# Optimization experiments

Hardware: AMD Instinct MI355X
Metric: run time of the kernel (lower is better)

The kernel has to match this reference:

```python
import jax, jax.numpy as jnp
import numpy as np


def setup_inputs() -> dict:
    key = jax.random.key(0)
    ks = jax.random.split(key, 5)
    B, S, C = 512, 512, 96
    emissions = jax.random.normal(ks[0], (B, S, C), dtype=jnp.float32)
    tags = jax.random.randint(ks[1], (B, S), 0, C, dtype=jnp.int64)
    masks = jnp.ones((B, S), dtype=bool)
    start_transitions = jax.random.uniform(ks[2], (C,), jnp.float32, -0.1, 0.1)
    end_transitions = jax.random.uniform(ks[3], (C,), jnp.float32, -0.1, 0.1)
    transitions = jax.random.uniform(ks[4], (C, C), jnp.float32, -0.1, 0.1)
    return {
        "emissions": emissions,
        "tags": tags,
        "masks": masks,
        "start_transitions": start_transitions,
        "end_transitions": end_transitions,
        "transitions": transitions,
    }


def _crf_llh(emissions, tags, masks, start_transitions, end_transitions, transitions):
    # to time-major: (S, B, C), (S, B)
    emissions = jnp.swapaxes(emissions, 0, 1)
    tags = jnp.swapaxes(tags, 0, 1)
    masks = jnp.swapaxes(masks, 0, 1)
    S, B, C = emissions.shape
    maskf = masks.astype(emissions.dtype)

    # ---- numerator: score of the gold tag path (fully vectorized over time) ----
    em_scores = jnp.take_along_axis(emissions, tags[:, :, None], axis=2)[:, :, 0]  # (S, B)
    trans_scores = transitions[tags[:-1], tags[1:]]  # (S-1, B)
    score = start_transitions[tags[0]] + em_scores[0]
    score = score + jnp.sum((trans_scores + em_scores[1:]) * maskf[1:], axis=0)
    seq_ends = masks.astype(jnp.int32).sum(axis=0) - 1  # (B,)
    last_tags = tags[seq_ends, jnp.arange(B)]
    numerator = score + end_transitions[last_tags]

    # ---- denominator: forward algorithm (sequential logsumexp recurrence) ----
    alpha0 = start_transitions[None, :] + emissions[0]  # (B, C)

    def step(alpha, inp):
        em_i, m_i = inp  # (B, C), (B,)
        # (B, C_prev, C_next)
        scores = alpha[:, :, None] + transitions[None, :, :] + em_i[:, None, :]
        next_alpha = jax.scipy.special.logsumexp(scores, axis=1)
        alpha = jnp.where(m_i[:, None], next_alpha, alpha)
        return alpha, None

    alpha, _ = jax.lax.scan(step, alpha0, (emissions[1:], masks[1:]))
    denominator = jax.scipy.special.logsumexp(alpha + end_transitions[None, :], axis=1)

    return jnp.mean(numerator - denominator)


def reference(emissions, tags, masks, start_transitions, end_transitions, transitions):
    return _crf_llh(emissions, tags, masks, start_transitions, end_transitions, transitions)
```

## Files before the change

kernel.cpp:

```cpp
#include <hip/hip_runtime.h>
#include <hip/hip_bf16.h>
#include <math.h>


#define BATCH 512
#define SEQ   512
#define NC    96
#define NTHR  128
#define LN2   0.69314718055994531f

typedef __fp16 half2v __attribute__((ext_vector_type(2)));

#define BARRIER() asm volatile("s_waitcnt lgkmcnt(0)\n\ts_barrier" ::: "memory")

#define DPP_STEP_F(v, op, ctrl)                                              \
    v = op(v, __int_as_float(__builtin_amdgcn_update_dpp(                    \
            __float_as_int(v), __float_as_int(v), (ctrl), 0xf, 0xf, false)))

__device__ __forceinline__ float wave_max_all(float v) {
    DPP_STEP_F(v, fmaxf, 0x111);
    DPP_STEP_F(v, fmaxf, 0x112);
    DPP_STEP_F(v, fmaxf, 0x114);
    DPP_STEP_F(v, fmaxf, 0x118);
    DPP_STEP_F(v, fmaxf, 0x142);
    DPP_STEP_F(v, fmaxf, 0x143);
    return __int_as_float(__builtin_amdgcn_readlane(__float_as_int(v), 63));
}
__device__ __forceinline__ float fadd_(float a, float b) { return a + b; }
__device__ __forceinline__ float wave_sum_all(float v) {
    DPP_STEP_F(v, fadd_, 0x111);
    DPP_STEP_F(v, fadd_, 0x112);
    DPP_STEP_F(v, fadd_, 0x114);
    DPP_STEP_F(v, fadd_, 0x118);
    DPP_STEP_F(v, fadd_, 0x142);
    DPP_STEP_F(v, fadd_, 0x143);
    return __int_as_float(__builtin_amdgcn_readlane(__float_as_int(v), 63));
}

__global__ __launch_bounds__(NTHR, 1)
void crf_llh_kernel(const float* __restrict__ em,
                    const int*   __restrict__ tags,
                    const int*   __restrict__ masks,
                    const float* __restrict__ startT,
                    const float* __restrict__ endT,
                    const float* __restrict__ trans,
                    float*       __restrict__ out)
{
    const int b    = blockIdx.x;
    const int tid  = threadIdx.x;
    const int lane = tid & 63;
    const int wid  = tid >> 6;
    const bool active = (tid < NC);
    const int jc = active ? tid : 0;

    __shared__ __align__(16) __fp16 qsh[2][128];
    __shared__ float maxsh[2][2];
    __shared__ float redn[2], redm[2], redd[2];

    const float* em_b    = em    + (size_t)b * SEQ * NC;
    const int*   tags_b  = tags  + b * SEQ;
    const int*   masks_b = masks + b * SEQ;

    half2v ecol[48];
    #pragma unroll
    for (int k = 0; k < 48; ++k) {
        ecol[k] = __builtin_amdgcn_cvt_pkrtz(
            __expf(trans[(2 * k)     * NC + jc]),
            __expf(trans[(2 * k + 1) * NC + jc]));
    }

    const float al0 = startT[jc] + em_b[jc];
    {
        const float wm = wave_max_all(active ? al0 : -1e30f);
        if (lane == 0) maxsh[0][wid] = wm;
    }
    BARRIER();
    const float M0 = fmaxf(maxsh[0][0], maxsh[0][1]);
    float wreg = active ? __expf(al0 - M0) : 0.f;
    qsh[1][tid] = (__fp16)wreg;
    BARRIER();

    int K    = 1;
    int sumk = 0;

    float emA = em_b[1 * NC + jc];
    float emB = em_b[2 * NC + jc];
    float emC = em_b[3 * NC + jc];
    int mkA = masks_b[1], mkB = masks_b[2], mkC = masks_b[3];

    for (int s = 1; s < SEQ; ++s) {
        const int rb = s & 1;
        const int sp = (s + 3 < SEQ) ? (s + 3) : (SEQ - 1);
        const float emN = em_b[sp * NC + jc];
        const int   mkN = masks_b[sp];

        const uint4* q4p = reinterpret_cast<const uint4*>(&qsh[rb][0]);
        uint4 qv[12];
        #pragma unroll
        for (int t = 0; t < 12; ++t) qv[t] = q4p[t];

        float acc[6] = {0.f, 0.f, 0.f, 0.f, 0.f, 0.f};
        #pragma unroll
        for (int t = 0; t < 12; ++t) {
            const half2v qx = __builtin_bit_cast(half2v, qv[t].x);
            const half2v qy = __builtin_bit_cast(half2v, qv[t].y);
            const half2v qz = __builtin_bit_cast(half2v, qv[t].z);
            const half2v qw = __builtin_bit_cast(half2v, qv[t].w);
            acc[(4 * t + 0) % 6] = __builtin_amdgcn_fdot2(qx, ecol[4 * t + 0], acc[(4 * t + 0) % 6], false);
            acc[(4 * t + 1) % 6] = __builtin_amdgcn_fdot2(qy, ecol[4 * t + 1], acc[(4 * t + 1) % 6], false);
            acc[(4 * t + 2) % 6] = __builtin_amdgcn_fdot2(qz, ecol[4 * t + 2], acc[(4 * t + 2) % 6], false);
            acc[(4 * t + 3) % 6] = __builtin_amdgcn_fdot2(qw, ecol[4 * t + 3], acc[(4 * t + 3) % 6], false);
        }
        const float U = ((acc[0] + acc[1]) + (acc[2] + acc[3])) + (acc[4] + acc[5]);

        const float F = __expf(emA);
        float w = ldexpf(U, -(K + 6)) * F;
        if (!active) w = 0.f;
        w = mkA ? w : wreg;
        sumk += mkA ? (K + 6) : 0;
        wreg = w;

        const float wmx = wave_max_all(w);
        if (lane == 0) maxsh[rb][wid] = wmx;
        qsh[rb ^ 1][tid] = (__fp16)w;
        BARRIER();

        const float r = fmaxf(maxsh[rb][0], maxsh[rb][1]);
        K = (int)((__float_as_uint(r) >> 23) & 255u) - 126;

        emA = emB; emB = emC; emC = emN;
        mkA = mkB; mkB = mkC; mkC = mkN;
    }

    const float dv = active ? wreg * __expf(endT[jc]) : 0.f;
    {
        const float ws = wave_sum_all(dv);
        if (lane == 0) redd[wid] = ws;
    }
    __syncthreads();
    const float denom = M0 + (float)sumk * LN2 + __logf(redd[0] + redd[1]);

    float nsum = 0.f, msum = 0.f;
    #pragma unroll
    for (int kk = 0; kk < SEQ / NTHR; ++kk) {
        const int s  = tid + NTHR * kk;
        const int tg = tags_b[s];
        const int mk = masks_b[s];
        msum += mk ? 1.f : 0.f;
        if (s == 0) {
            nsum += startT[tg] + em_b[tg];
        } else if (mk) {
            nsum += trans[tags_b[s - 1] * NC + tg] + em_b[s * NC + tg];
        }
    }
    nsum = wave_sum_all(nsum);
    msum = wave_sum_all(msum);
    if (lane == 0) { redn[wid] = nsum; redm[wid] = msum; }
    __syncthreads();
    if (tid == 0) {
        const float numer = redn[0] + redn[1];
        const int   cnt   = (int)(redm[0] + redm[1]);
        const int   last  = tags_b[cnt - 1];
        atomicAdd(out, (numer + endT[last] - denom) * (1.0f / (float)BATCH));
    }
}

extern "C" void kernel_launch(void* const* d_in, const int* in_sizes, int n_in,
                              void* d_out, int out_size, void* d_ws, size_t ws_size,
                              hipStream_t stream) {
    const float* em     = (const float*)d_in[0];
    const int*   tags   = (const int*)  d_in[1];
    const int*   masks  = (const int*)  d_in[2];
    const float* startT = (const float*)d_in[3];
    const float* endT   = (const float*)d_in[4];
    const float* trans  = (const float*)d_in[5];
    float* out = (float*)d_out;

    (void)hipMemsetAsync(out, 0, sizeof(float), stream);
    crf_llh_kernel<<<BATCH, NTHR, 0, stream>>>(em, tags, masks, startT, endT, trans, out);
}
```

Measured before the change: 402.9 us.

## Fuse timestep pairs via MFMA-built two-step transition matrices in producer warps

Three producer waves use MFMA to build, for each pair of timesteps, the combined matrix E·diag(exp(em))·E in fp16 shared memory, double-buffered. A single consumer wave then applies one matvec per two steps, which halves the serial recurrence length. Masked steps fall back to single-step matvecs. This trades extra parallel MFMA work and fp16 precision loss in the fused matrix for a shorter sequential dependency chain and fewer barriers per step.

After: 426.3 us. 1.06x slower.

```diff
diff --git a/kernel.cpp b/kernel.cpp
--- a/kernel.cpp
+++ b/kernel.cpp
@@ -1,31 +1,28 @@
 #include <hip/hip_runtime.h>
-#include <hip/hip_bf16.h>
 #include <math.h>
 
 
 #define BATCH 512
 #define SEQ   512
 #define NC    96
-#define NTHR  128
+#define NTHR  256
+#define CSTR  120
+#define GHALF (NC * CSTR)
 #define LN2   0.69314718055994531f
 
 typedef __fp16 half2v __attribute__((ext_vector_type(2)));
+typedef __fp16 half8  __attribute__((ext_vector_type(8)));
+typedef float  f32x4  __attribute__((ext_vector_type(4)));
+typedef unsigned int uint2v __attribute__((ext_vector_type(2)));
+typedef unsigned int uint4v __attribute__((ext_vector_type(4)));
 
 #define BARRIER() asm volatile("s_waitcnt lgkmcnt(0)\n\ts_barrier" ::: "memory")
+#define LGKM0()   asm volatile("s_waitcnt lgkmcnt(0)" ::: "memory")
 
 #define DPP_STEP_F(v, op, ctrl)                                              \
     v = op(v, __int_as_float(__builtin_amdgcn_update_dpp(                    \
             __float_as_int(v), __float_as_int(v), (ctrl), 0xf, 0xf, false)))
 
-__device__ __forceinline__ float wave_max_all(float v) {
-    DPP_STEP_F(v, fmaxf, 0x111);
-    DPP_STEP_F(v, fmaxf, 0x112);
-    DPP_STEP_F(v, fmaxf, 0x114);
-    DPP_STEP_F(v, fmaxf, 0x118);
-    DPP_STEP_F(v, fmaxf, 0x142);
-    DPP_STEP_F(v, fmaxf, 0x143);
-    return __int_as_float(__builtin_amdgcn_readlane(__float_as_int(v), 63));
-}
 __device__ __forceinline__ float fadd_(float a, float b) { return a + b; }
 __device__ __forceinline__ float wave_sum_all(float v) {
     DPP_STEP_F(v, fadd_, 0x111);
@@ -36,132 +33,274 @@
     DPP_STEP_F(v, fadd_, 0x143);
     return __int_as_float(__builtin_amdgcn_readlane(__float_as_int(v), 63));
 }
-
-__global__ __launch_bounds__(NTHR, 1)
-void crf_llh_kernel(const float* __restrict__ em,
-                    const int*   __restrict__ tags,
-                    const int*   __restrict__ masks,
-                    const float* __restrict__ startT,
-                    const float* __restrict__ endT,
-                    const float* __restrict__ trans,
-                    float*       __restrict__ out)
+__device__ __forceinline__ float wave_max_all(float v) {
+    DPP_STEP_F(v, fmaxf, 0x111);
+    DPP_STEP_F(v, fmaxf, 0x112);
+    DPP_STEP_F(v, fmaxf, 0x114);
+    DPP_STEP_F(v, fmaxf, 0x118);
+    DPP_STEP_F(v, fmaxf, 0x142);
+    DPP_STEP_F(v, fmaxf, 0x143);
+    return __int_as_float(__builtin_amdgcn_readlane(__float_as_int(v), 63));
+}
+
+__device__ __forceinline__ unsigned bcu(half2v h) { return __builtin_bit_cast(unsigned, h); }
+__device__ __forceinline__ half2v bch(unsigned u) { return __builtin_bit_cast(half2v, u); }
+__device__ __forceinline__ float fdot2_(unsigned a, unsigned b, float c) {
+    return __builtin_amdgcn_fdot2(bch(a), bch(b), c, false);
+}
+
+__device__ __forceinline__ void matvec96(const __fp16* base, const __fp16* st,
+                                         int jj, float& u0, float& u1) {
+    const uint4v* c0 = (const uint4v*)(base + (2 * jj) * CSTR);
+    const uint4v* c1 = (const uint4v*)(base + (2 * jj) * CSTR + CSTR);
+    const uint4v* sp = (const uint4v*)st;
+    uint4v g0[12], g1[12], sv[12];
+    #pragma unroll
+    for (int q = 0; q < 12; ++q) g0[q] = c0[q];
+    #pragma unroll
+    for (int q = 0; q < 12; ++q) g1[q] = c1[q];
+    #pragma unroll
+    for (int q = 0; q < 12; ++q) sv[q] = sp[q];
+    float a0 = 0.f, a1 = 0.f, a2 = 0.f, a3 = 0.f;
+    float b0 = 0.f, b1 = 0.f, b2 = 0.f, b3 = 0.f;
+    #pragma unroll
+    for (int q = 0; q < 12; ++q) {
+        a0 = fdot2_(sv[q].x, g0[q].x, a0);
+        a1 = fdot2_(sv[q].y, g0[q].y, a1);
+        a2 = fdot2_(sv[q].z, g0[q].z, a2);
+        a3 = fdot2_(sv[q].w, g0[q].w, a3);
+        b0 = fdot2_(sv[q].x, g1[q].x, b0);
+        b1 = fdot2_(sv[q].y, g1[q].y, b1);
+        b2 = fdot2_(sv[q].z, g1[q].z, b2);
+        b3 = fdot2_(sv[q].w, g1[q].w, b3);
+    }
+    u0 = (a0 + a1) + (a2 + a3);
+    u1 = (b0 + b1) + (b2 + b3);
+}
+
+struct PF { float4 a0, a1, b0, b1, c0, c1; };
+
+__device__ __forceinline__ PF ld6(const float* p_base, int row, int g) {
+    const float* p = p_base + (size_t)row * NC + 8 * g;
+    PF x;
+    x.a0 = *(const float4*)(p);      x.a1 = *(const float4*)(p + 4);
+    x.b0 = *(const float4*)(p + 32); x.b1 = *(const float4*)(p + 36);
+    x.c0 = *(const float4*)(p + 64); x.c1 = *(const float4*)(p + 68);
+    return x;
+}
+
+__device__ __forceinline__ half8 exp8(float4 u, float4 v) {
+    uint4v r;
+    r.x = bcu(__builtin_amdgcn_cvt_pkrtz(__expf(u.x), __expf(u.y)));
+    r.y = bcu(__builtin_amdgcn_cvt_pkrtz(__expf(u.z), __expf(u.w)));
+    r.z = bcu(__builtin_amdgcn_cvt_pkrtz(__expf(v.x), __expf(v.y)));
+    r.w = bcu(__builtin_amdgcn_cvt_pkrtz(__expf(v.z), __expf(v.w)));
+    return __builtin_bit_cast(half8, r);
+}
+
+__global__ __launch_bounds__(NTHR, 2)
+void crf_pair_kernel(const float* __restrict__ em,
+                     const int*   __restrict__ tags,
+                     const int*   __restrict__ masks,
+                     const float* __restrict__ startT,
+                     const float* __restrict__ endT,
+                     const float* __restrict__ trans,
+                     float*       __restrict__ out)
 {
-    const int b    = blockIdx.x;
-    const int tid  = threadIdx.x;
-    const int lane = tid & 63;
-    const int wid  = tid >> 6;
-    const bool active = (tid < NC);
-    const int jc = active ? tid : 0;
-
-    __shared__ __align__(16) __fp16 qsh[2][128];
-    __shared__ float maxsh[2][2];
-    __shared__ float redn[2], redm[2], redd[2];
+    const int tid = threadIdx.x;
+    const int l   = tid & 63;
+    const int w   = tid >> 6;
+    const int b   = blockIdx.x;
+
+    __shared__ __align__(16) __fp16 GB[2][GHALF];
+    __shared__ __align__(16) __fp16 EB[GHALF];
+    __shared__ __align__(16) __fp16 ST[128];
 
     const float* em_b    = em    + (size_t)b * SEQ * NC;
-    const int*   tags_b  = tags  + b * SEQ;
-    const int*   masks_b = masks + b * SEQ;
-
-    half2v ecol[48];
-    #pragma unroll
-    for (int k = 0; k < 48; ++k) {
-        ecol[k] = __builtin_amdgcn_cvt_pkrtz(
-            __expf(trans[(2 * k)     * NC + jc]),
-            __expf(trans[(2 * k + 1) * NC + jc]));
-    }
-
-    const float al0 = startT[jc] + em_b[jc];
-    {
-        const float wm = wave_max_all(active ? al0 : -1e30f);
-        if (lane == 0) maxsh[0][wid] = wm;
-    }
-    BARRIER();
-    const float M0 = fmaxf(maxsh[0][0], maxsh[0][1]);
-    float wreg = active ? __expf(al0 - M0) : 0.f;
-    qsh[1][tid] = (__fp16)wreg;
-    BARRIER();
-
-    int K    = 1;
-    int sumk = 0;
-
-    float emA = em_b[1 * NC + jc];
-    float emB = em_b[2 * NC + jc];
-    float emC = em_b[3 * NC + jc];
-    int mkA = masks_b[1], mkB = masks_b[2], mkC = masks_b[3];
-
-    for (int s = 1; s < SEQ; ++s) {
-        const int rb = s & 1;
-        const int sp = (s + 3 < SEQ) ? (s + 3) : (SEQ - 1);
-        const float emN = em_b[sp * NC + jc];
-        const int   mkN = masks_b[sp];
-
-        const uint4* q4p = reinterpret_cast<const uint4*>(&qsh[rb][0]);
-        uint4 qv[12];
+    const int*   masks_b = masks + (size_t)b * SEQ;
+
+    if (w == 0) {
+        const int jj = (l < 48) ? l : (l - 48);
+
+        const float2 st2 = *(const float2*)(startT + 2 * jj);
+        const float2 e00 = *(const float2*)(em_b + 2 * jj);
+        const float al0 = st2.x + e00.x, al1 = st2.y + e00.y;
+        const float M0 = wave_max_all(fmaxf(al0, al1));
+        if (l < 48)
+            ((unsigned*)ST)[jj] = bcu(__builtin_amdgcn_cvt_pkrtz(
+                __expf(al0 - M0), __expf(al1 - M0)));
+        int sk = 0;
+
+        float2 e2A = *(const float2*)(em_b + (size_t)2 * NC + 2 * jj);
+        float2 e2B = *(const float2*)(em_b + (size_t)4 * NC + 2 * jj);
+        int mkA = (masks_b[1] ? 1 : 0) | (masks_b[2] ? 2 : 0);
+        int mkB = (masks_b[3] ? 1 : 0) | (masks_b[4] ? 2 : 0);
+
+        auto sstep = [&](int row) {
+            LGKM0();
+            float v0, v1;
+            matvec96(EB, ST, jj, v0, v1);
+            const float2 ee = *(const float2*)(em_b + (size_t)row * NC + 2 * jj);
+            v0 *= __expf(ee.x); v1 *= __expf(ee.y);
+            const float mx = wave_max_all(fmaxf(v0, v1));
+            const unsigned ebx = (__float_as_uint(mx) >> 23) & 255u;
+            sk += (int)ebx - 127;
+            const float sc = __uint_as_float((254u - ebx) << 23);
+            if (l < 48)
+                ((unsigned*)ST)[jj] = bcu(__builtin_amdgcn_cvt_pkrtz(v0 * sc, v1 * sc));
+            LGKM0();
+        };
+
+        auto body = [&](int t, float2 e2, int mk) {
+            BARRIER();
+            float u0, u1;
+            matvec96(&GB[t & 1][0], ST, jj, u0, u1);
+            if (mk == 3) {
+                u0 *= __expf(e2.x); u1 *= __expf(e2.y);
+                const float mx = wave_max_all(fmaxf(u0, u1));
+                const unsigned ebx = (__float_as_uint(mx) >> 23) & 255u;
+                sk += (int)ebx - 127;
+                const float sc = __uint_as_float((254u - ebx) << 23);
+                if (l < 48)
+                    ((unsigned*)ST)[jj] = bcu(__builtin_amdgcn_cvt_pkrtz(u0 * sc, u1 * sc));
+            } else {
+                if (mk & 1) sstep(2 * t + 1);
+                if (mk & 2) sstep(2 * t + 2);
+            }
+        };
+
+        #pragma unroll 1
+        for (int t = 0; t < 254; t += 2) {
+            body(t, e2A, mkA);
+            {
+                const int rb = 2 * t + 6;
+                e2A = *(const float2*)(em_b + (size_t)rb * NC + 2 * jj);
+                mkA = (masks_b[2 * t + 5] ? 1 : 0) | (masks_b[rb] ? 2 : 0);
+            }
+            body(t + 1, e2B, mkB);
+            {
+                const int ra = 2 * t + 7;
+                const int rb = (2 * t + 8 > 511) ? 511 : (2 * t + 8);
+                e2B = *(const float2*)(em_b + (size_t)rb * NC + 2 * jj);
+                mkB = (masks_b[ra] ? 1 : 0) | (masks_b[rb] ? 2 : 0);
+            }
+        }
+        body(254, e2A, mkA);
+
+        LGKM0();
+        float u0, u1;
+        matvec96(EB, ST, jj, u0, u1);
+        const float2 e5 = *(const float2*)(em_b + (size_t)511 * NC + 2 * jj);
+        if (masks_b[511]) { u0 *= __expf(e5.x); u1 *= __expf(e5.y); }
+        else { u0 = (float)ST[2 * jj]; u1 = (float)ST[2 * jj + 1]; }
+        const float2 en = *(const float2*)(endT + 2 * jj);
+        const float dvl = (l < 48) ? (u0 * __expf(en.x) + u1 * __expf(en.y)) : 0.f;
+        const float dv = wave_sum_all(dvl);
+        if (l == 0)
+            atomicAdd(out, -(M0 + (float)sk * LN2 + __logf(dv)) * (1.0f / (float)BATCH));
+    } else {
+        const int lidx = l & 15;
+        const int g    = l >> 4;
+        const int nt0  = 2 * (w - 1);
+
+        half8 Ea[6][3];
         #pragma unroll
-        for (int t = 0; t < 12; ++t) qv[t] = q4p[t];
-
-        float acc[6] = {0.f, 0.f, 0.f, 0.f, 0.f, 0.f};
+        for (int r = 0; r < 6; ++r)
+            #pragma unroll
+            for (int c = 0; c < 3; ++c) {
+                half8 v;
+                #pragma unroll
+                for (int e = 0; e < 8; ++e)
+                    v[e] = (__fp16)__expf(trans[(16 * r + lidx) * NC + 32 * c + 8 * g + e]);
+                Ea[r][c] = v;
+            }
+        half8 Eb[3][2];
         #pragma unroll
-        for (int t = 0; t < 12; ++t) {
-            const half2v qx = __builtin_bit_cast(half2v, qv[t].x);
-            const half2v qy = __builtin_bit_cast(half2v, qv[t].y);
-            const half2v qz = __builtin_bit_cast(half2v, qv[t].z);
-            const half2v qw = __builtin_bit_cast(half2v, qv[t].w);
-            acc[(4 * t + 0) % 6] = __builtin_amdgcn_fdot2(qx, ecol[4 * t + 0], acc[(4 * t + 0) % 6], false);
-            acc[(4 * t + 1) % 6] = __builtin_amdgcn_fdot2(qy, ecol[4 * t + 1], acc[(4 * t + 1) % 6], false);
-            acc[(4 * t + 2) % 6] = __builtin_amdgcn_fdot2(qz, ecol[4 * t + 2], acc[(4 * t + 2) % 6], false);
-            acc[(4 * t + 3) % 6] = __builtin_amdgcn_fdot2(qw, ecol[4 * t + 3], acc[(4 * t + 3) % 6], false);
+        for (int c = 0; c < 3; ++c)
+            #pragma unroll
+            for (int ntL = 0; ntL < 2; ++ntL) {
+                half8 v;
+                #pragma unroll
+                for (int e = 0; e < 8; ++e)
+                    v[e] = (__fp16)__expf(trans[(32 * c + 8 * g + e) * NC + 16 * (nt0 + ntL) + lidx]);
+                Eb[c][ntL] = v;
+            }
+        #pragma unroll
+        for (int ntL = 0; ntL < 2; ++ntL)
+            #pragma unroll
+            for (int c = 0; c < 3; ++c)
+                *(uint4v*)(EB + (16 * (nt0 + ntL) + lidx) * CSTR + 32 * c + 8 * g) =
+                    __builtin_bit_cast(uint4v, Eb[c][ntL]);
+
+        auto build = [&](int bsel, const PF& pf) {
+            half8 d0 = exp8(pf.a0, pf.a1);
+            half8 d1 = exp8(pf.b0, pf.b1);
+            half8 d2 = exp8(pf.c0, pf.c1);
+            half8 bw[3][2];
+            #pragma unroll
+            for (int ntL = 0; ntL < 2; ++ntL) {
+                bw[0][ntL] = Eb[0][ntL] * d0;
+                bw[1][ntL] = Eb[1][ntL] * d1;
+                bw[2][ntL] = Eb[2][ntL] * d2;
+            }
+            __fp16* dst = &GB[bsel][0];
+            #pragma unroll
+            for (int ntL = 0; ntL < 2; ++ntL) {
+                #pragma unroll
+                for (int r = 0; r < 6; ++r) {
+                    const f32x4 z = {0.f, 0.f, 0.f, 0.f};
+                    f32x4 acc = __builtin_amdgcn_mfma_f32_16x16x32_f16(Ea[r][0], bw[0][ntL], z, 0, 0, 0);
+                    acc = __builtin_amdgcn_mfma_f32_16x16x32_f16(Ea[r][1], bw[1][ntL], acc, 0, 0, 0);
+                    acc = __builtin_amdgcn_mfma_f32_16x16x32_f16(Ea[r][2], bw[2][ntL], acc, 0, 0, 0);
+                    uint2v wv;
+                    wv.x = bcu(__builtin_amdgcn_cvt_pkrtz(acc[0], acc[1]));
+                    wv.y = bcu(__builtin_amdgcn_cvt_pkrtz(acc[2], acc[3]));
+                    *(uint2v*)(dst + (16 * (nt0 + ntL) + lidx) * CSTR + 16 * r + 4 * g) = wv;
+                }
+            }
+        };
+
+        {
+            const PF p0 = ld6(em_b, 1, g);
+            build(0, p0);
         }
-        const float U = ((acc[0] + acc[1]) + (acc[2] + acc[3])) + (acc[4] + acc[5]);
-
-        const float F = __expf(emA);
-        float w = ldexpf(U, -(K + 6)) * F;
-        if (!active) w = 0.f;
-        w = mkA ? w : wreg;
-        sumk += mkA ? (K + 6) : 0;
-        wreg = w;
-
-        const float wmx = wave_max_all(w);
-        if (lane == 0) maxsh[rb][wid] = wmx;
-        qsh[rb ^ 1][tid] = (__fp16)w;
+        PF r0 = ld6(em_b, 3, g);
+        PF r1 = ld6(em_b, 5, g);
+
+        #pragma unroll 1
+        for (int t = 0; t < 254; t += 2) {
+            BARRIER();
+            build(1, r0);
+            { const int rr = 2 * t + 7; r0 = ld6(em_b, rr > 511 ? 511 : rr, g); }
+            BARRIER();
+            build(0, r1);
+            { const int rr = 2 * t + 9; r1 = ld6(em_b, rr > 511 ? 511 : rr, g); }
+        }
         BARRIER();
 
-        const float r = fmaxf(maxsh[rb][0], maxsh[rb][1]);
-        K = (int)((__float_as_uint(r) >> 23) & 255u) - 126;
-
-        emA = emB; emB = emC; emC = emN;
-        mkA = mkB; mkB = mkC; mkC = mkN;
-    }
-
-    const float dv = active ? wreg * __expf(endT[jc]) : 0.f;
-    {
-        const float ws = wave_sum_all(dv);
-        if (lane == 0) redd[wid] = ws;
-    }
-    __syncthreads();
-    const float denom = M0 + (float)sumk * LN2 + __logf(redd[0] + redd[1]);
-
-    float nsum = 0.f, msum = 0.f;
-    #pragma unroll
-    for (int kk = 0; kk < SEQ / NTHR; ++kk) {
-        const int s  = tid + NTHR * kk;
-        const int tg = tags_b[s];
-        const int mk = masks_b[s];
-        msum += mk ? 1.f : 0.f;
-        if (s == 0) {
-            nsum += startT[tg] + em_b[tg];
-        } else if (mk) {
-            nsum += trans[tags_b[s - 1] * NC + tg] + em_b[s * NC + tg];
+        if (w == 1) {
+            const int* tb = tags + (size_t)b * SEQ;
+            float nsum = 0.f, msum = 0.f;
+            #pragma unroll
+            for (int kk = 0; kk < 8; ++kk) {
+                const int s  = l + 64 * kk;
+                const int tg = tb[s];
+                const int mk = masks_b[s];
+                msum += mk ? 1.f : 0.f;
+                if (s == 0) {
+                    nsum += startT[tg] + em_b[tg];
+                } else if (mk) {
+                    nsum += trans[tb[s - 1] * NC + tg] + em_b[(size_t)s * NC + tg];
+                }
+            }
+            nsum = wave_sum_all(nsum);
+            msum = wave_sum_all(msum);
+            if (l == 0) {
+                const int cnt  = (int)msum;
+                const int last = tb[cnt - 1];
+                atomicAdd(out, (nsum + endT[last]) * (1.0f / (float)BATCH));
+            }
         }
-    }
-    nsum = wave_sum_all(nsum);
-    msum = wave_sum_all(msum);
-    if (lane == 0) { redn[wid] = nsum; redm[wid] = msum; }
-    __syncthreads();
-    if (tid == 0) {
-        const float numer = redn[0] + redn[1];
-        const int   cnt   = (int)(redm[0] + redm[1]);
-        const int   last  = tags_b[cnt - 1];
-        atomicAdd(out, (numer + endT[last] - denom) * (1.0f / (float)BATCH));
     }
 }
 
@@ -177,5 +316,5 @@
     float* out = (float*)d_out;
 
     (void)hipMemsetAsync(out, 0, sizeof(float), stream);
-    crf_llh_kernel<<<BATCH, NTHR, 0, stream>>>(em, tags, masks, startT, endT, trans, out);
-}
+    crf_pair_kernel<<<BATCH, NTHR, 0, stream>>>(em, tags, masks, startT, endT, trans, out);
+}
```
